# Kernel optimization log

Hardware: AMD Instinct MI355X
Metric: run time of the kernel (lower is better)

Reference implementation:

```python
import math
import jax, jax.numpy as jnp
import numpy as np

B, S, D = 4, 2048, 1024
NEG = -1e20

def setup_inputs() -> dict:
    key = jax.random.key(0)
    k1, k2, k3, k4 = jax.random.split(key, 4)
    X = jax.random.normal(k1, (B, S, D), dtype=jnp.float32)
    # True = masked position (masked_fill semantics)
    attention_mask = jax.random.randint(k2, (B, S, S), 0, 2).astype(bool)
    scale = 1.0 / math.sqrt(D)
    W_qkv = jax.random.normal(k3, (D, 3 * D), dtype=jnp.float32) * scale
    b_qkv = jnp.zeros((3 * D,), dtype=jnp.float32)
    W_out = jax.random.normal(k4, (D, D), dtype=jnp.float32) * scale
    b_out = jnp.zeros((D,), dtype=jnp.float32)
    return {"X": X, "attention_mask": attention_mask,
            "W_qkv": W_qkv, "b_qkv": b_qkv, "W_out": W_out, "b_out": b_out}

def reference(X, attention_mask, W_qkv, b_qkv, W_out, b_out):
    dim = X.shape[-1]
    QKV = X @ W_qkv + b_qkv                      # [B,S,3D]
    Q, K, V = jnp.split(QKV, 3, axis=-1)         # each [B,S,D]
    scores = jnp.einsum('bqd,bkd->bqk', Q, K) / math.sqrt(dim)  # [B,S,S]
    scores = jnp.where(attention_mask, NEG, scores)
    attn = jax.nn.softmax(scores, axis=-1)       # dropout_rate=0.0 -> identity
    ctx = jnp.einsum('bqk,bkd->bqd', attn, V)    # [B,S,D]
    return ctx @ W_out + b_out
```

## Files before the change

kernel.cpp:

```cpp
#include <hip/hip_runtime.h>
#include <cstdint>
#include <cstddef>

#define BB 4
#define SS 2048
#define DD 1024

typedef _Float16 f16;
typedef _Float16 f16x8 __attribute__((ext_vector_type(8)));
typedef _Float16 f16x4 __attribute__((ext_vector_type(4)));
typedef float fx4 __attribute__((ext_vector_type(4)));

__device__ __forceinline__ void async_copy16(void* lds, const void* g) {
  __builtin_amdgcn_global_load_lds(
      (__attribute__((address_space(1))) void*)const_cast<void*>(g),
      (__attribute__((address_space(3))) void*)lds,
      16, 0, 0);
}

enum { EPI_BIAS = 0, EPI_MASKEXP = 1, EPI_ROWSCALE = 2 };

template <typename OutT, int MODE>
__global__ __launch_bounds__(256, 2) void gemm_nt(
    const f16* __restrict__ A, long long strideA, int lda,
    const f16* __restrict__ Bt, long long strideB, int ldb,
    OutT* __restrict__ C, long long strideC, int ldc,
    const float* __restrict__ bias, const int* __restrict__ mask,
    float* __restrict__ rowSum, float scale, int K) {
  __shared__ __align__(16) char smem[16384];
  f16* As = (f16*)smem;
  f16* Bs = (f16*)(smem + 8192);

  const int t = threadIdx.x;
  const int lane = t & 63;
  const int wid = t >> 6;
  const long long bz = blockIdx.z;
  const int tileM = blockIdx.y * 128;
  const int tileN = blockIdx.x * 128;

  const f16* Ab = A + bz * strideA;
  const f16* Bb = Bt + bz * strideB;
  OutT* Cb = C + bz * strideC;

  const int sr = t >> 2;
  const int sc = (((t & 3) ^ ((t >> 3) & 3)) * 8);
  const f16* pa0 = Ab + (size_t)(tileM + sr) * lda + sc;
  const f16* pa1 = Ab + (size_t)(tileM + 64 + sr) * lda + sc;
  const f16* pb0 = Bb + (size_t)(tileN + sr) * ldb + sc;
  const f16* pb1 = Bb + (size_t)(tileN + 64 + sr) * ldb + sc;
  f16* la0 = &As[t * 8];
  f16* la1 = &As[2048 + t * 8];
  f16* lb0 = &Bs[t * 8];
  f16* lb1 = &Bs[2048 + t * 8];

  const int waveM = (wid >> 1) * 64;
  const int waveN = (wid & 1) * 64;
  const int r16 = lane & 15;
  const int quad = lane >> 4;
  const int sw = (r16 >> 1) & 3;

  fx4 acc[4][4] = {};

  for (int k0 = 0; k0 < K; k0 += 32) {
    async_copy16(la0, pa0 + k0);
    async_copy16(la1, pa1 + k0);
    async_copy16(lb0, pb0 + k0);
    async_copy16(lb1, pb1 + k0);
    __syncthreads();

    f16x8 af[4], bf[4];
#pragma unroll
    for (int i = 0; i < 4; ++i)
      af[i] = *(const f16x8*)&As[(waveM + i * 16 + r16) * 32 + (quad ^ sw) * 8];
#pragma unroll
    for (int i = 0; i < 4; ++i)
      bf[i] = *(const f16x8*)&Bs[(waveN + i * 16 + r16) * 32 + (quad ^ sw) * 8];

#pragma unroll
    for (int i = 0; i < 4; ++i)
#pragma unroll
      for (int j = 0; j < 4; ++j)
        acc[i][j] =
            __builtin_amdgcn_mfma_f32_16x16x32_f16(af[i], bf[j], acc[i][j], 0, 0, 0);
    __syncthreads();
  }

  if constexpr (MODE == EPI_BIAS) {
#pragma unroll
    for (int j = 0; j < 4; ++j) {
      const int col = tileN + waveN + j * 16 + r16;
      const float bv = bias[col];
#pragma unroll
      for (int i = 0; i < 4; ++i) {
#pragma unroll
        for (int r = 0; r < 4; ++r) {
          const int row = tileM + waveM + i * 16 + quad * 4 + r;
          Cb[(size_t)row * ldc + col] = (OutT)(acc[i][j][r] * scale + bv);
        }
      }
    }
  } else if constexpr (MODE == EPI_MASKEXP) {
    uint8_t* lm = (uint8_t*)smem;
    const int* maskb = mask + bz * (long long)SS * SS;
#pragma unroll
    for (int it = 0; it < 16; ++it) {
      const int f = it * 256 + t;
      const int r = f >> 5;
      const int q = f & 31;
      const int4 mv =
          *(const int4*)&maskb[(size_t)(tileM + r) * SS + tileN + q * 4];
      uchar4 mb;
      mb.x = mv.x ? 1 : 0;
      mb.y = mv.y ? 1 : 0;
      mb.z = mv.z ? 1 : 0;
      mb.w = mv.w ? 1 : 0;
      const int c4 = (q * 4) ^ (((r >> 2) & 3) * 32);
      *(uchar4*)&lm[r * 128 + c4] = mb;
    }
    __syncthreads();

#pragma unroll
    for (int i = 0; i < 4; ++i) {
#pragma unroll
      for (int r = 0; r < 4; ++r) {
        const int lr = waveM + i * 16 + quad * 4 + r;
        const int row = tileM + lr;
        const int swm = ((lr >> 2) & 3) * 32;
        float part = 0.0f;
#pragma unroll
        for (int j = 0; j < 4; ++j) {
          const int lc = waveN + j * 16 + r16;
          const int mv = lm[lr * 128 + (lc ^ swm)];
          const float e = mv ? 0.0f : __expf(acc[i][j][r] * scale);
          Cb[(size_t)row * ldc + tileN + lc] = (OutT)e;
          part += e;
        }
#pragma unroll
        for (int d = 1; d < 16; d <<= 1) part += __shfl_xor(part, d, 64);
        if (r16 == 0) atomicAdd(&rowSum[bz * SS + row], part);
      }
    }
  } else {
#pragma unroll
    for (int i = 0; i < 4; ++i) {
#pragma unroll
      for (int r = 0; r < 4; ++r) {
        const int row = tileM + waveM + i * 16 + quad * 4 + r;
        const float inv = scale / rowSum[bz * SS + row];
#pragma unroll
        for (int j = 0; j < 4; ++j) {
          const int col = tileN + waveN + j * 16 + r16;
          Cb[(size_t)row * ldc + col] = (OutT)(acc[i][j][r] * inv);
        }
      }
    }
  }
}

__global__ __launch_bounds__(256) void k_conv(const float* __restrict__ in,
                                              f16* __restrict__ out, int n4) {
  const int i = blockIdx.x * 256 + threadIdx.x;
  if (i >= n4) return;
  const float4 v = ((const float4*)in)[i];
  f16x4 h = {(f16)v.x, (f16)v.y, (f16)v.z, (f16)v.w};
  ((f16x4*)out)[i] = h;
}

__global__ __launch_bounds__(256) void k_zero(float* __restrict__ p, int n) {
  const int i = blockIdx.x * 256 + threadIdx.x;
  if (i < n) p[i] = 0.0f;
}

__global__ __launch_bounds__(256) void k_transpose_conv(const float* __restrict__ in,
                                                        f16* __restrict__ out, int R,
                                                        int C) {
  __shared__ float tile[32][33];
  const int bx = blockIdx.x * 32;
  const int by = blockIdx.y * 32;
  const int tx = threadIdx.x;
  const int ty = threadIdx.y;
  for (int i = ty; i < 32; i += 8)
    tile[i][tx] = in[(size_t)(by + i) * C + bx + tx];
  __syncthreads();
  for (int i = ty; i < 32; i += 8)
    out[(size_t)(bx + i) * R + by + tx] = (f16)tile[tx][i];
}

__global__ __launch_bounds__(256) void k_transpose_h(const f16* __restrict__ in,
                                                     long long strideIn, int ldin,
                                                     int R, f16* __restrict__ out,
                                                     long long strideOut) {
  const int b = blockIdx.z;
  in += (long long)b * strideIn;
  out += (long long)b * strideOut;
  __shared__ f16 tile[32][33];
  const int bx = blockIdx.x * 32;
  const int by = blockIdx.y * 32;
  const int tx = threadIdx.x;
  const int ty = threadIdx.y;
  for (int i = ty; i < 32; i += 8)
    tile[i][tx] = in[(size_t)(by + i) * ldin + bx + tx];
  __syncthreads();
  for (int i = ty; i < 32; i += 8)
    out[(size_t)(bx + i) * R + by + tx] = tile[tx][i];
}

extern "C" void kernel_launch(void* const* d_in, const int* in_sizes, int n_in,
                              void* d_out, int out_size, void* d_ws, size_t ws_size,
                              hipStream_t stream) {
  const float* X = (const float*)d_in[0];
  const int* mask = (const int*)d_in[1];
  const float* Wqkv = (const float*)d_in[2];
  const float* bqkv = (const float*)d_in[3];
  const float* Wout = (const float*)d_in[4];
  const float* bout = (const float*)d_in[5];
  float* out = (float*)d_out;

  char* ws = (char*)d_ws;
  f16* Xh = (f16*)(ws + 0);
  f16* Wqkvt = (f16*)(ws + 16777216);
  f16* Woutt = (f16*)(ws + 23068672);
  f16* QKV = (f16*)(ws + 25165824);
  f16* Vt = (f16*)(ws + 75497472);
  f16* E = (f16*)(ws + 92274688);
  f16* Ctx = (f16*)(ws + 125829120);
  float* rowSum = (float*)(ws + 142606336);

  k_conv<<<dim3(8192), dim3(256), 0, stream>>>(X, Xh, 8388608 / 4);
  k_transpose_conv<<<dim3(96, 32), dim3(32, 8), 0, stream>>>(Wqkv, Wqkvt, DD, 3 * DD);
  k_transpose_conv<<<dim3(32, 32), dim3(32, 8), 0, stream>>>(Wout, Woutt, DD, DD);
  k_zero<<<dim3(32), dim3(256), 0, stream>>>(rowSum, BB * SS);

  gemm_nt<f16, EPI_BIAS><<<dim3(24, 64, 1), dim3(256), 0, stream>>>(
      Xh, 0LL, DD, Wqkvt, 0LL, DD, QKV, 0LL, 3 * DD, bqkv, nullptr, nullptr, 1.0f, DD);

  k_transpose_h<<<dim3(32, 64, 4), dim3(32, 8), 0, stream>>>(
      QKV + 2 * DD, (long long)SS * 3 * DD, 3 * DD, SS, Vt, (long long)DD * SS);

  gemm_nt<f16, EPI_MASKEXP><<<dim3(16, 16, 4), dim3(256), 0, stream>>>(
      QKV, (long long)SS * 3 * DD, 3 * DD, QKV + DD, (long long)SS * 3 * DD, 3 * DD,
      E, (long long)SS * SS, SS, nullptr, mask, rowSum, 0.03125f, DD);

  gemm_nt<f16, EPI_ROWSCALE><<<dim3(8, 16, 4), dim3(256), 0, stream>>>(
      E, (long long)SS * SS, SS, Vt, (long long)DD * SS, SS, Ctx,
      (long long)SS * DD, DD, nullptr, nullptr, rowSum, 1.0f, SS);

  gemm_nt<float, EPI_BIAS><<<dim3(8, 64, 1), dim3(256), 0, stream>>>(
      Ctx, 0LL, DD, Woutt, 0LL, DD, out, 0LL, DD, bout, nullptr, nullptr, 1.0f, DD);
}
```

Measured before the change: 366.9 us.

## Double-buffer GEMM LDS tiles and write V transposed from QKV epilogue

The GEMM main loop now uses two LDS buffers. It issues the async global-to-LDS loads for the next K slice before computing the current one, which removes one barrier per iteration and overlaps loads with MFMA work. The QKV projection gains a new epilogue that writes Q and K into a compact 2D-wide buffer and stores V directly in transposed layout. This removes the separate transpose kernel and the extra pass over V. In exchange, LDS per block doubles to 32KB, which may limit occupancy, and the transposed V stores are strided 8-byte writes.

```diff
diff --git a/kernel.cpp b/kernel.cpp
--- a/kernel.cpp
+++ b/kernel.cpp
@@ -18,7 +18,7 @@
       16, 0, 0);
 }
 
-enum { EPI_BIAS = 0, EPI_MASKEXP = 1, EPI_ROWSCALE = 2 };
+enum { EPI_BIAS = 0, EPI_MASKEXP = 1, EPI_ROWSCALE = 2, EPI_QKV = 3 };
 
 template <typename OutT, int MODE>
 __global__ __launch_bounds__(256, 2) void gemm_nt(
@@ -26,10 +26,8 @@
     const f16* __restrict__ Bt, long long strideB, int ldb,
     OutT* __restrict__ C, long long strideC, int ldc,
     const float* __restrict__ bias, const int* __restrict__ mask,
-    float* __restrict__ rowSum, float scale, int K) {
-  __shared__ __align__(16) char smem[16384];
-  f16* As = (f16*)smem;
-  f16* Bs = (f16*)(smem + 8192);
+    float* __restrict__ rowSum, f16* __restrict__ vt, float scale, int K) {
+  __shared__ __align__(16) char smem[32768];
 
   const int t = threadIdx.x;
   const int lane = t & 63;
@@ -48,10 +46,7 @@
   const f16* pa1 = Ab + (size_t)(tileM + 64 + sr) * lda + sc;
   const f16* pb0 = Bb + (size_t)(tileN + sr) * ldb + sc;
   const f16* pb1 = Bb + (size_t)(tileN + 64 + sr) * ldb + sc;
-  f16* la0 = &As[t * 8];
-  f16* la1 = &As[2048 + t * 8];
-  f16* lb0 = &Bs[t * 8];
-  f16* lb1 = &Bs[2048 + t * 8];
+  const int tb = t * 16;
 
   const int waveM = (wid >> 1) * 64;
   const int waveN = (wid & 1) * 64;
@@ -61,28 +56,43 @@
 
   fx4 acc[4][4] = {};
 
-  for (int k0 = 0; k0 < K; k0 += 32) {
-    async_copy16(la0, pa0 + k0);
-    async_copy16(la1, pa1 + k0);
-    async_copy16(lb0, pb0 + k0);
-    async_copy16(lb1, pb1 + k0);
+  const int nIter = K >> 5;
+  {
+    char* b0 = smem;
+    async_copy16(b0 + tb, pa0);
+    async_copy16(b0 + 4096 + tb, pa1);
+    async_copy16(b0 + 8192 + tb, pb0);
+    async_copy16(b0 + 12288 + tb, pb1);
+  }
+
+#pragma unroll 2
+  for (int i = 0; i < nIter; ++i) {
     __syncthreads();
+    if (i + 1 < nIter) {
+      char* nb = smem + ((i + 1) & 1) * 16384;
+      const int k = (i + 1) << 5;
+      async_copy16(nb + tb, pa0 + k);
+      async_copy16(nb + 4096 + tb, pa1 + k);
+      async_copy16(nb + 8192 + tb, pb0 + k);
+      async_copy16(nb + 12288 + tb, pb1 + k);
+    }
+    const f16* As = (const f16*)(smem + (i & 1) * 16384);
+    const f16* Bs = As + 4096;
 
     f16x8 af[4], bf[4];
 #pragma unroll
-    for (int i = 0; i < 4; ++i)
-      af[i] = *(const f16x8*)&As[(waveM + i * 16 + r16) * 32 + (quad ^ sw) * 8];
-#pragma unroll
-    for (int i = 0; i < 4; ++i)
-      bf[i] = *(const f16x8*)&Bs[(waveN + i * 16 + r16) * 32 + (quad ^ sw) * 8];
-
-#pragma unroll
-    for (int i = 0; i < 4; ++i)
+    for (int x = 0; x < 4; ++x)
+      af[x] = *(const f16x8*)&As[(waveM + x * 16 + r16) * 32 + (quad ^ sw) * 8];
+#pragma unroll
+    for (int x = 0; x < 4; ++x)
+      bf[x] = *(const f16x8*)&Bs[(waveN + x * 16 + r16) * 32 + (quad ^ sw) * 8];
+
+#pragma unroll
+    for (int x = 0; x < 4; ++x)
 #pragma unroll
       for (int j = 0; j < 4; ++j)
-        acc[i][j] =
-            __builtin_amdgcn_mfma_f32_16x16x32_f16(af[i], bf[j], acc[i][j], 0, 0, 0);
-    __syncthreads();
+        acc[x][j] =
+            __builtin_amdgcn_mfma_f32_16x16x32_f16(af[x], bf[j], acc[x][j], 0, 0, 0);
   }
 
   if constexpr (MODE == EPI_BIAS) {
@@ -96,6 +106,40 @@
         for (int r = 0; r < 4; ++r) {
           const int row = tileM + waveM + i * 16 + quad * 4 + r;
           Cb[(size_t)row * ldc + col] = (OutT)(acc[i][j][r] * scale + bv);
+        }
+      }
+    }
+  } else if constexpr (MODE == EPI_QKV) {
+    if (tileN < 2 * DD) {
+#pragma unroll
+      for (int j = 0; j < 4; ++j) {
+        const int col = tileN + waveN + j * 16 + r16;
+        const float bv = bias[col];
+#pragma unroll
+        for (int i = 0; i < 4; ++i) {
+#pragma unroll
+          for (int r = 0; r < 4; ++r) {
+            const int row = tileM + waveM + i * 16 + quad * 4 + r;
+            Cb[(size_t)row * ldc + col] = (OutT)(acc[i][j][r] + bv);
+          }
+        }
+      }
+    } else {
+      const int b = tileM >> 11;
+      const int s0 = (tileM & 2047) + waveM;
+      f16* vb = vt + (size_t)b * DD * SS;
+#pragma unroll
+      for (int j = 0; j < 4; ++j) {
+        const int col = tileN + waveN + j * 16 + r16;
+        const float bv = bias[col];
+        const int d = col - 2 * DD;
+#pragma unroll
+        for (int i = 0; i < 4; ++i) {
+          const int s = s0 + i * 16 + quad * 4;
+          f16x4 v4;
+#pragma unroll
+          for (int r = 0; r < 4; ++r) v4[r] = (f16)(acc[i][j][r] + bv);
+          *(f16x4*)&vb[(size_t)d * SS + s] = v4;
         }
       }
     }
@@ -186,25 +230,6 @@
     out[(size_t)(bx + i) * R + by + tx] = (f16)tile[tx][i];
 }
 
-__global__ __launch_bounds__(256) void k_transpose_h(const f16* __restrict__ in,
-                                                     long long strideIn, int ldin,
-                                                     int R, f16* __restrict__ out,
-                                                     long long strideOut) {
-  const int b = blockIdx.z;
-  in += (long long)b * strideIn;
-  out += (long long)b * strideOut;
-  __shared__ f16 tile[32][33];
-  const int bx = blockIdx.x * 32;
-  const int by = blockIdx.y * 32;
-  const int tx = threadIdx.x;
-  const int ty = threadIdx.y;
-  for (int i = ty; i < 32; i += 8)
-    tile[i][tx] = in[(size_t)(by + i) * ldin + bx + tx];
-  __syncthreads();
-  for (int i = ty; i < 32; i += 8)
-    out[(size_t)(bx + i) * R + by + tx] = tile[tx][i];
-}
-
 extern "C" void kernel_launch(void* const* d_in, const int* in_sizes, int n_in,
                               void* d_out, int out_size, void* d_ws, size_t ws_size,
                               hipStream_t stream) {
@@ -220,31 +245,30 @@
   f16* Xh = (f16*)(ws + 0);
   f16* Wqkvt = (f16*)(ws + 16777216);
   f16* Woutt = (f16*)(ws + 23068672);
-  f16* QKV = (f16*)(ws + 25165824);
-  f16* Vt = (f16*)(ws + 75497472);
-  f16* E = (f16*)(ws + 92274688);
-  f16* Ctx = (f16*)(ws + 125829120);
-  float* rowSum = (float*)(ws + 142606336);
+  f16* QK = (f16*)(ws + 25165824);
+  f16* Vt = (f16*)(ws + 58720256);
+  f16* E = (f16*)(ws + 75497472);
+  f16* Ctx = (f16*)(ws + 109051904);
+  float* rowSum = (float*)(ws + 125829120);
 
   k_conv<<<dim3(8192), dim3(256), 0, stream>>>(X, Xh, 8388608 / 4);
   k_transpose_conv<<<dim3(96, 32), dim3(32, 8), 0, stream>>>(Wqkv, Wqkvt, DD, 3 * DD);
   k_transpose_conv<<<dim3(32, 32), dim3(32, 8), 0, stream>>>(Wout, Woutt, DD, DD);
   k_zero<<<dim3(32), dim3(256), 0, stream>>>(rowSum, BB * SS);
 
-  gemm_nt<f16, EPI_BIAS><<<dim3(24, 64, 1), dim3(256), 0, stream>>>(
-      Xh, 0LL, DD, Wqkvt, 0LL, DD, QKV, 0LL, 3 * DD, bqkv, nullptr, nullptr, 1.0f, DD);
-
-  k_transpose_h<<<dim3(32, 64, 4), dim3(32, 8), 0, stream>>>(
-      QKV + 2 * DD, (long long)SS * 3 * DD, 3 * DD, SS, Vt, (long long)DD * SS);
+  gemm_nt<f16, EPI_QKV><<<dim3(24, 64, 1), dim3(256), 0, stream>>>(
+      Xh, 0LL, DD, Wqkvt, 0LL, DD, QK, 0LL, 2 * DD, bqkv, nullptr, nullptr, Vt,
+      1.0f, DD);
 
   gemm_nt<f16, EPI_MASKEXP><<<dim3(16, 16, 4), dim3(256), 0, stream>>>(
-      QKV, (long long)SS * 3 * DD, 3 * DD, QKV + DD, (long long)SS * 3 * DD, 3 * DD,
-      E, (long long)SS * SS, SS, nullptr, mask, rowSum, 0.03125f, DD);
+      QK, (long long)SS * 2 * DD, 2 * DD, QK + DD, (long long)SS * 2 * DD, 2 * DD,
+      E, (long long)SS * SS, SS, nullptr, mask, rowSum, nullptr, 0.03125f, DD);
 
   gemm_nt<f16, EPI_ROWSCALE><<<dim3(8, 16, 4), dim3(256), 0, stream>>>(
       E, (long long)SS * SS, SS, Vt, (long long)DD * SS, SS, Ctx,
-      (long long)SS * DD, DD, nullptr, nullptr, rowSum, 1.0f, SS);
+      (long long)SS * DD, DD, nullptr, nullptr, rowSum, nullptr, 1.0f, SS);
 
   gemm_nt<float, EPI_BIAS><<<dim3(8, 64, 1), dim3(256), 0, stream>>>(
-      Ctx, 0LL, DD, Woutt, 0LL, DD, out, 0LL, DD, bout, nullptr, nullptr, 1.0f, DD);
-}
+      Ctx, 0LL, DD, Woutt, 0LL, DD, out, 0LL, DD, bout, nullptr, nullptr, nullptr,
+      1.0f, DD);
+}
```

After: 356.3 us. 2.9% less time.
